# Kernel tuning notes

Measured on AMD Instinct MI355X. Metric: run time of the kernel, lower is better.

Reference implementation:

```python
import jax, jax.numpy as jnp
import numpy as np

N, LQ, D_MODEL, M_HEADS, P_POINTS, H_DIM, W_DIM = 8, 4096, 256, 8, 4, 64, 64


def setup_inputs() -> dict:
    key = jax.random.key(0)
    ks = jax.random.split(key, 9)
    d = D_MODEL
    scale = 1.0 / np.sqrt(d).astype(np.float32)
    return {
        "query": jax.random.normal(ks[0], (N, LQ, d), jnp.float32),
        "reference_points": jax.random.uniform(ks[1], (N, LQ, 2), jnp.float32),
        "input_flatten": jax.random.normal(ks[2], (N, H_DIM * W_DIM, d), jnp.float32),
        "H": H_DIM,
        "W": W_DIM,
        "Wv": jax.random.normal(ks[3], (d, d), jnp.float32) * scale,
        "bv": jnp.zeros((d,), jnp.float32),
        "Woff": jax.random.normal(ks[4], (M_HEADS * P_POINTS * 2, d), jnp.float32) * 0.01,
        "boff": jax.random.normal(ks[5], (M_HEADS * P_POINTS * 2,), jnp.float32) * 0.5,
        "Wa": jax.random.normal(ks[6], (M_HEADS * P_POINTS, d), jnp.float32) * 0.01,
        "ba": jnp.zeros((M_HEADS * P_POINTS,), jnp.float32),
        "Wo": jax.random.normal(ks[7], (d, d), jnp.float32) * scale,
        "bo": jnp.zeros((d,), jnp.float32),
    }


def _bilinear_sample(val, grid, H, W):
    # val: [B, D, H*W]; grid: [B, Lq, P, 2] in [-1, 1] (x, y); align_corners=False, zero padding.
    B, D, _ = val.shape
    _, Lq, P, _ = grid.shape
    x = (grid[..., 0] + 1.0) * (W * 0.5) - 0.5
    y = (grid[..., 1] + 1.0) * (H * 0.5) - 0.5
    x0 = jnp.floor(x)
    y0 = jnp.floor(y)
    x0i = x0.astype(jnp.int32)
    y0i = y0.astype(jnp.int32)
    wx1 = x - x0
    wy1 = y - y0
    out = jnp.zeros((B, D, Lq, P), val.dtype)
    for xi, wx in ((x0i, 1.0 - wx1), (x0i + 1, wx1)):
        for yi, wy in ((y0i, 1.0 - wy1), (y0i + 1, wy1)):
            valid = (xi >= 0) & (xi < W) & (yi >= 0) & (yi < H)
            idx = jnp.clip(yi, 0, H - 1) * W + jnp.clip(xi, 0, W - 1)  # [B, Lq, P]
            g = jnp.take_along_axis(val, idx.reshape(B, 1, Lq * P), axis=2).reshape(B, D, Lq, P)
            w = jnp.where(valid, wx * wy, 0.0)
            out = out + g * w[:, None]
    return out


def reference(query, reference_points, input_flatten, H, W, Wv, bv, Woff, boff, Wa, ba, Wo, bo):
    n, lq, d = query.shape
    m, p = M_HEADS, P_POINTS
    dh = d // m
    value = (input_flatten @ Wv.T + bv).reshape(n, H * W, m, dh)
    offsets = (query @ Woff.T + boff).reshape(n, lq, m, p, 2)
    attw = jax.nn.softmax((query @ Wa.T + ba).reshape(n, lq, m, p), axis=-1)
    normalizer = jnp.array([W, H], dtype=query.dtype)  # [W, H] order per torch code
    loc = reference_points[:, :, None, None, :] + offsets / normalizer
    grid = 2.0 * loc - 1.0  # [n, lq, m, p, 2]
    # value -> [n*m, dh, H*W] matching torch flatten(2).transpose(1,2).reshape
    val = jnp.transpose(value, (0, 2, 3, 1)).reshape(n * m, dh, H * W)
    grd = jnp.transpose(grid, (0, 2, 1, 3, 4)).reshape(n * m, lq, p, 2)
    samp = _bilinear_sample(val, grd, H, W)  # [n*m, dh, lq, p]
    aw = jnp.transpose(attw, (0, 2, 1, 3)).reshape(n * m, 1, lq, p)
    out = (samp * aw).sum(-1).reshape(n, m * dh, lq)
    out = jnp.transpose(out, (0, 2, 1))  # [n, lq, d]
    return out @ Wo.T + bo
```

## Files before the change

### kernel.cpp

```cpp
#include <hip/hip_runtime.h>
#include <math.h>

#define NB   8
#define LQN  4096
#define DM   256
#define MH   8
#define PP   4
#define HH   64
#define WW   64
#define PW   67
#define PPIX (PW*PW)

typedef __bf16 bf16x8 __attribute__((ext_vector_type(8)));
typedef float  f32x4  __attribute__((ext_vector_type(4)));
typedef unsigned short us8 __attribute__((ext_vector_type(8)));
typedef unsigned short us4 __attribute__((ext_vector_type(4)));

__device__ __forceinline__ unsigned short f2bf(float f) {
    unsigned u = __float_as_uint(f);
    u += 0x7FFFu + ((u >> 16) & 1u);
    return (unsigned short)(u >> 16);
}
__device__ __forceinline__ float bf2f(unsigned short b) {
    return __uint_as_float((unsigned)b << 16);
}

__device__ __forceinline__ void gl2lds16(const void* g, unsigned short* l) {
    __builtin_amdgcn_global_load_lds(
        (const __attribute__((address_space(1))) void*)g,
        (__attribute__((address_space(3))) void*)l,
        16, 0, 0);
}

__device__ __forceinline__ bf16x8 cvt_frag(const unsigned short* s, int row, int kq) {
    const int u0 = row * 8 + ((kq * 2) ^ (row & 7));
    const int u1 = u0 ^ 1;
    const f32x4 a0 = *(const f32x4*)&s[u0 * 8];
    const f32x4 a1 = *(const f32x4*)&s[u1 * 8];
    bf16x8 v;
    v[0] = (__bf16)a0[0]; v[1] = (__bf16)a0[1];
    v[2] = (__bf16)a0[2]; v[3] = (__bf16)a0[3];
    v[4] = (__bf16)a1[0]; v[5] = (__bf16)a1[1];
    v[6] = (__bf16)a1[2]; v[7] = (__bf16)a1[3];
    return v;
}

__global__ __launch_bounds__(256)
void prep_kernel(const float* __restrict__ Wv, const float* __restrict__ Wo,
                 const float* __restrict__ Woff, const float* __restrict__ Wa,
                 const float* __restrict__ boff, const float* __restrict__ ba,
                 unsigned short* __restrict__ Wvh, unsigned short* __restrict__ Woh,
                 unsigned short* __restrict__ Wcath, float* __restrict__ bcat,
                 unsigned short* __restrict__ valueP) {
    const int i = blockIdx.x * 256 + threadIdx.x;
    if (i < 65536) {
        Wvh[i] = f2bf(Wv[i]);
    } else if (i < 131072) {
        const int j = i - 65536;
        Woh[j] = f2bf(Wo[j]);
    } else if (i < 163840) {
        const int j = i - 131072, n = j >> 8, k = j & 255;
        const float v = (n < 64) ? Woff[n * 256 + k]
                                 : ((n < 96) ? Wa[(n - 64) * 256 + k] : 0.f);
        Wcath[j] = f2bf(v);
    } else if (i < 163968) {
        const int n = i - 163840;
        bcat[n] = (n < 64) ? boff[n] : ((n < 96) ? ba[n - 64] : 0.f);
    } else if (i < 163968 + 201216) {
        const int j   = i - 163968;
        const int c4  = j & 63;
        const int pix = j >> 6;
        const int n   = pix / 393;
        const int r   = pix - n * 393;
        int x, y;
        if (r < 201) {
            const int q = r / 67;
            y = (q == 0) ? 0 : (q == 1 ? 65 : 66);
            x = r - q * 67;
        } else {
            const int q = r - 201;
            y = 1 + q / 3;
            const int s = q - (q / 3) * 3;
            x = (s == 0) ? 0 : (s == 1 ? 65 : 66);
        }
        const size_t addr = ((size_t)n * PPIX + (size_t)y * PW + x) * DM + c4 * 4;
        *(ushort4*)&valueP[addr] = make_ushort4(0, 0, 0, 0);
    }
}

__global__ __launch_bounds__(256, 4)
void value_gemm(const float* __restrict__ Ain,
                const unsigned short* __restrict__ Wvh,
                const float* __restrict__ bv,
                unsigned short* __restrict__ valueP) {
    constexpr int K = 256, NK = 8;
    __shared__ unsigned short sA[2][4096];
    __shared__ unsigned short sB[2][4096];

    const int t   = threadIdx.x;
    const int blk = blockIdx.x;
    const int xb  = blk & 7;
    const int idx = blk >> 3;
    const int brow = xb * 4096 + (idx >> 1) * 64;
    const int bcol = (idx & 1) * 128;

    const int srow = t >> 3;
    const int scq  = (t & 7) ^ (srow & 7);
    const float* aG = Ain + (size_t)(brow + srow) * K + scq * 4;
    const size_t aI = (size_t)32 * K;

    const unsigned short* bG = Wvh + (size_t)(bcol + (t >> 2)) * K + (t & 3) * 8;
    const size_t bI = (size_t)64 * K;

    const int l   = t & 63;
    const int wid = t >> 6;
    const int wr  = wid >> 1, wc = wid & 1;
    const int fr  = l & 15,   kq = l >> 4;

    f32x4 acc[2][4] = {};

#define STAGE(buf, ks_) { const int k0_ = (ks_) * 32;                    \
       gl2lds16(aG + k0_,      &sA[buf][t * 8]);                         \
       gl2lds16(aG + k0_ + aI, &sA[buf][2048 + t * 8]);                  \
       gl2lds16(bG + k0_,      &sB[buf][t * 8]);                         \
       gl2lds16(bG + k0_ + bI, &sB[buf][2048 + t * 8]); }

    STAGE(0, 0);
    STAGE(1, 1);

    for (int ks = 0; ks < NK; ++ks) {
        const int cur = ks & 1;
        if (ks < NK - 1) asm volatile("s_waitcnt vmcnt(4)" ::: "memory");
        else             asm volatile("s_waitcnt vmcnt(0)" ::: "memory");
        __builtin_amdgcn_s_barrier();
        __builtin_amdgcn_sched_barrier(0);

        bf16x8 af[2], bf_[4];
#pragma unroll
        for (int m = 0; m < 2; ++m)
            af[m]  = cvt_frag(sA[cur], wr * 32 + m * 16 + fr, kq);
#pragma unroll
        for (int n = 0; n < 4; ++n)
            bf_[n] = *(const bf16x8*)&sB[cur][(wc * 64 + n * 16 + fr) * 32 + kq * 8];

#pragma unroll
        for (int m = 0; m < 2; ++m)
#pragma unroll
            for (int n = 0; n < 4; ++n)
                acc[m][n] = __builtin_amdgcn_mfma_f32_16x16x32_bf16(
                    bf_[n], af[m], acc[m][n], 0, 0, 0);

        __builtin_amdgcn_sched_barrier(0);
        __builtin_amdgcn_s_barrier();
        if (ks + 2 < NK) STAGE(cur, ks + 2);
    }
#undef STAGE

#pragma unroll
    for (int m = 0; m < 2; ++m) {
        const int row = brow + wr * 32 + m * 16 + fr;
        const int nb_ = row >> 12;
        const int pix = row & 4095;
        const int y   = pix >> 6, x = pix & 63;
        const size_t rbase =
            ((size_t)nb_ * PPIX + (size_t)(y + 1) * PW + (x + 1)) * DM;
#pragma unroll
        for (int n = 0; n < 4; ++n) {
            const int colq = bcol + wc * 64 + n * 16 + kq * 4;
            const float4 b4 = *(const float4*)&bv[colq];
            us4 o;
            o[0] = f2bf(acc[m][n][0] + b4.x);
            o[1] = f2bf(acc[m][n][1] + b4.y);
            o[2] = f2bf(acc[m][n][2] + b4.z);
            o[3] = f2bf(acc[m][n][3] + b4.w);
            *(us4*)&valueP[rbase + colq] = o;
        }
    }
}

__global__ __launch_bounds__(512, 4)
void fused_lso(const float* __restrict__ query, const float* __restrict__ refp,
               const unsigned short* __restrict__ valueP,
               const unsigned short* __restrict__ Wcath,
               const float* __restrict__ bcat,
               const unsigned short* __restrict__ Woh,
               const float* __restrict__ bo, float* __restrict__ C) {
    constexpr int K = 256, NK = 8;
    extern __shared__ unsigned short smem[];
    unsigned short* sS = smem;
    unsigned short* sB = smem + 16384;
    unsigned short* sL = smem + 32768;

    const int t    = threadIdx.x;
    const int blk  = blockIdx.x;
    const int nb   = blk & 7;
    const int brow = nb * 4096 + (blk >> 3) * 64;
    const int w    = t >> 6;
    const int lane = t & 63;
    const int fr   = lane & 15, kq = lane >> 4;

    {
        unsigned short* sQ = sS;
        unsigned short* sW = sS + 8192;

        const int srow = t >> 3;
        const int scq  = (t & 7) ^ (srow & 7);
        const float* aG = query + (size_t)(brow + srow) * K + scq * 4;
        const unsigned short* wG = Wcath + (size_t)(t >> 2) * K + (t & 3) * 8;

        const int wr0 = w >> 2;
        const int wc0 = w & 3;

        f32x4 acc[2][2] = {};

#define STG0(buf, ks_) { const int k0_ = (ks_) * 32;                     \
       gl2lds16(aG + k0_, &sQ[(buf) * 4096 + t * 8]);                    \
       gl2lds16(wG + k0_, &sW[(buf) * 4096 + t * 8]); }

        STG0(0, 0);
        STG0(1, 1);

        for (int ks = 0; ks < NK; ++ks) {
            const int cur = ks & 1;
            if (ks < NK - 1) asm volatile("s_waitcnt vmcnt(2)" ::: "memory");
            else             asm volatile("s_waitcnt vmcnt(0)" ::: "memory");
            __builtin_amdgcn_s_barrier();
            __builtin_amdgcn_sched_barrier(0);

            bf16x8 af[2], bw[2];
#pragma unroll
            for (int m = 0; m < 2; ++m)
                af[m] = cvt_frag(&sQ[cur * 4096], wr0 * 32 + m * 16 + fr, kq);
#pragma unroll
            for (int n = 0; n < 2; ++n)
                bw[n] = *(const bf16x8*)&sW[cur * 4096 +
                        (wc0 * 32 + n * 16 + fr) * 32 + kq * 8];

#pragma unroll
            for (int m = 0; m < 2; ++m)
#pragma unroll
                for (int n = 0; n < 2; ++n)
                    acc[m][n] = __builtin_amdgcn_mfma_f32_16x16x32_bf16(
                        bw[n], af[m], acc[m][n], 0, 0, 0);

            __builtin_amdgcn_sched_barrier(0);
            __builtin_amdgcn_s_barrier();
            if (ks + 2 < NK) STG0(cur, ks + 2);
        }
#undef STG0

#pragma unroll
        for (int m = 0; m < 2; ++m) {
            const int row = wr0 * 32 + m * 16 + fr;
#pragma unroll
            for (int n = 0; n < 2; ++n) {
                const int colq = wc0 * 32 + n * 16 + kq * 4;
                const float4 b4 = *(const float4*)&bcat[colq];
                us4 o;
                o[0] = f2bf(acc[m][n][0] + b4.x);
                o[1] = f2bf(acc[m][n][1] + b4.y);
                o[2] = f2bf(acc[m][n][2] + b4.z);
                o[3] = f2bf(acc[m][n][3] + b4.w);
                *(us4*)&sL[row * 128 + colq] = o;
            }
        }
    }
    __syncthreads();

    {
        const int tp  = lane & 31;
        const int pm  = tp >> 2, ppt = tp & 3;
        const int half = lane >> 5;
        const int c8   = lane & 31;
        const int mh   = c8 >> 2;
        const unsigned short* vbase = valueP + (size_t)nb * (PPIX * DM) + c8 * 8;

        for (int i = 0; i < 8; ++i) {
            const int q = w * 8 + i;
            const int b = brow + q;
            const unsigned short* lg = sL + q * 128;

            const float rx = refp[(size_t)b * 2 + 0];
            const float ry = refp[(size_t)b * 2 + 1];
            const float ox = bf2f(lg[pm * 8 + ppt * 2 + 0]);
            const float oy = bf2f(lg[pm * 8 + ppt * 2 + 1]);
            const float la = bf2f(lg[64 + tp]);

            const float x = fminf(fmaxf(fmaf(rx, (float)WW, ox) - 0.5f, -1.0f), 64.0f);
            const float y = fminf(fmaxf(fmaf(ry, (float)HH, oy) - 0.5f, -1.0f), 64.0f);

            float mx = fmaxf(la, __shfl_xor(la, 1));
            mx = fmaxf(mx, __shfl_xor(mx, 2));
            const float e = __expf(la - mx);
            float den = e + __shfl_xor(e, 1);
            den += __shfl_xor(den, 2);
            const float wgt = e / den;

            float accv[8] = {};
#pragma unroll
            for (int p = 0; p < PP; ++p) {
                const int   sl = mh * PP + p;
                const float xp = __shfl(x, sl);
                const float yp = __shfl(y, sl);
                const float wp = __shfl(wgt, sl);

                const float x0f = floorf(xp), y0f = floorf(yp);
                const int   x0 = (int)x0f,   y0 = (int)y0f;
                const float wx1 = xp - x0f,  wy1 = yp - y0f;
                const float wy  = half ? wy1 : (1.f - wy1);
                const float wA  = wp * wy * (1.f - wx1);
                const float wB  = wp * wy * wx1;

                const unsigned short* p0 =
                    vbase + (size_t)((y0 + 1 + half) * PW + (x0 + 1)) * DM;
                const us8 gA = *(const us8*)(p0);
                const us8 gB = *(const us8*)(p0 + DM);
#pragma unroll
                for (int j = 0; j < 8; ++j) {
                    accv[j] = fmaf(wA, bf2f(gA[j]), accv[j]);
                    accv[j] = fmaf(wB, bf2f(gB[j]), accv[j]);
                }
            }
#pragma unroll
            for (int j = 0; j < 8; ++j)
                accv[j] += __shfl_xor(accv[j], 32);

            if (half == 0) {
                us8 o;
#pragma unroll
                for (int j = 0; j < 8; ++j) o[j] = f2bf(accv[j]);
                *(us8*)&sS[q * 256 + ((c8 ^ (q & 7)) * 8)] = o;
            }
        }
    }
    __syncthreads();

    const unsigned short* bG = Woh + (size_t)(t >> 2) * K + (t & 3) * 8;
    const size_t rHalf = (size_t)128 * K;

    const int wr = w >> 2, wc = w & 3;

    f32x4 acc[2][4] = {};

#define STAGEF(buf, ks_) { const int k0_ = (ks_) * 32;                   \
       gl2lds16(bG + k0_,         &sB[(buf) * 8192 + t * 8]);            \
       gl2lds16(bG + k0_ + rHalf, &sB[(buf) * 8192 + 4096 + t * 8]); }

    STAGEF(0, 0);
    STAGEF(1, 1);

    for (int ks = 0; ks < NK; ++ks) {
        const int cur = ks & 1;
        if (ks < NK - 1) asm volatile("s_waitcnt vmcnt(2)" ::: "memory");
        else             asm volatile("s_waitcnt vmcnt(0)" ::: "memory");
        __builtin_amdgcn_s_barrier();
        __builtin_amdgcn_sched_barrier(0);

        bf16x8 af[2], bfr[4];
#pragma unroll
        for (int m = 0; m < 2; ++m) {
            const int row = wr * 32 + m * 16 + fr;
            const int u   = (ks * 4 + kq) ^ (row & 7);
            af[m] = *(const bf16x8*)&sS[row * 256 + u * 8];
        }
#pragma unroll
        for (int n = 0; n < 4; ++n)
            bfr[n] = *(const bf16x8*)&sB[cur * 8192 + (wc * 64 + n * 16 + fr) * 32 + kq * 8];

#pragma unroll
        for (int m = 0; m < 2; ++m)
#pragma unroll
            for (int n = 0; n < 4; ++n)
                acc[m][n] = __builtin_amdgcn_mfma_f32_16x16x32_bf16(
                    bfr[n], af[m], acc[m][n], 0, 0, 0);

        __builtin_amdgcn_sched_barrier(0);
        __builtin_amdgcn_s_barrier();
        if (ks + 2 < NK) STAGEF(cur, ks + 2);
    }
#undef STAGEF

#pragma unroll
    for (int m = 0; m < 2; ++m) {
        const int row = brow + wr * 32 + m * 16 + fr;
#pragma unroll
        for (int n = 0; n < 4; ++n) {
            const int colq = wc * 64 + n * 16 + kq * 4;
            const float4 bs = *(const float4*)&bo[colq];
            float4 o;
            o.x = acc[m][n][0] + bs.x; o.y = acc[m][n][1] + bs.y;
            o.z = acc[m][n][2] + bs.z; o.w = acc[m][n][3] + bs.w;
            *(float4*)&C[(size_t)row * DM + colq] = o;
        }
    }
}

extern "C" void kernel_launch(void* const* d_in, const int* in_sizes, int n_in,
                              void* d_out, int out_size, void* d_ws, size_t ws_size,
                              hipStream_t stream) {
    const float* query  = (const float*)d_in[0];
    const float* refp   = (const float*)d_in[1];
    const float* inputf = (const float*)d_in[2];
    const float* Wv   = (const float*)d_in[5];
    const float* bv   = (const float*)d_in[6];
    const float* Woff = (const float*)d_in[7];
    const float* boff = (const float*)d_in[8];
    const float* Wa   = (const float*)d_in[9];
    const float* ba   = (const float*)d_in[10];
    const float* Wo   = (const float*)d_in[11];
    const float* bo   = (const float*)d_in[12];
    float* out = (float*)d_out;

    unsigned short* valueP = (unsigned short*)d_ws;
    unsigned short* Wvh    = valueP + (size_t)NB * PPIX * DM;
    unsigned short* Woh    = Wvh    + 65536;
    unsigned short* Wcath  = Woh    + 65536;
    float*          bcat   = (float*)(Wcath + 32768);

    prep_kernel<<<1427, 256, 0, stream>>>(Wv, Wo, Woff, Wa, boff, ba,
                                          Wvh, Woh, Wcath, bcat, valueP);

    value_gemm<<<1024, 256, 0, stream>>>(inputf, Wvh, bv, valueP);

    fused_lso<<<512, 512, 81920, stream>>>(query, refp, valueP, Wcath, bcat,
                                           Woh, bo, out);
}
```

Baseline: 59.14 us.

## Halve rows per block and load GEMM operands directly from global memory

The fused kernel now handles 32 query rows per block instead of 64 and launches 1024 blocks. The projection and output GEMMs drop their LDS double-buffered staging and instead read query and weight fragments straight from global memory into MFMA registers, which shrinks dynamic shared memory from 80 KB to 24 KB. The aim is higher occupancy and fewer barriers. In exchange, weight tiles are re-read from global or L2 by more blocks, and uncoalesced per-lane fragment loads replace the staged copies.

```diff
diff --git a/kernel.cpp b/kernel.cpp
--- a/kernel.cpp
+++ b/kernel.cpp
@@ -185,84 +185,52 @@
                const float* __restrict__ bcat,
                const unsigned short* __restrict__ Woh,
                const float* __restrict__ bo, float* __restrict__ C) {
-    constexpr int K = 256, NK = 8;
     extern __shared__ unsigned short smem[];
     unsigned short* sS = smem;
-    unsigned short* sB = smem + 16384;
-    unsigned short* sL = smem + 32768;
+    unsigned short* sL = smem + 8192;
 
     const int t    = threadIdx.x;
     const int blk  = blockIdx.x;
     const int nb   = blk & 7;
-    const int brow = nb * 4096 + (blk >> 3) * 64;
+    const int brow = nb * 4096 + (blk >> 3) * 32;
     const int w    = t >> 6;
     const int lane = t & 63;
     const int fr   = lane & 15, kq = lane >> 4;
 
     {
-        unsigned short* sQ = sS;
-        unsigned short* sW = sS + 8192;
-
-        const int srow = t >> 3;
-        const int scq  = (t & 7) ^ (srow & 7);
-        const float* aG = query + (size_t)(brow + srow) * K + scq * 4;
-        const unsigned short* wG = Wcath + (size_t)(t >> 2) * K + (t & 3) * 8;
-
         const int wr0 = w >> 2;
         const int wc0 = w & 3;
-
-        f32x4 acc[2][2] = {};
-
-#define STG0(buf, ks_) { const int k0_ = (ks_) * 32;                     \
-       gl2lds16(aG + k0_, &sQ[(buf) * 4096 + t * 8]);                    \
-       gl2lds16(wG + k0_, &sW[(buf) * 4096 + t * 8]); }
-
-        STG0(0, 0);
-        STG0(1, 1);
-
-        for (int ks = 0; ks < NK; ++ks) {
-            const int cur = ks & 1;
-            if (ks < NK - 1) asm volatile("s_waitcnt vmcnt(2)" ::: "memory");
-            else             asm volatile("s_waitcnt vmcnt(0)" ::: "memory");
-            __builtin_amdgcn_s_barrier();
-            __builtin_amdgcn_sched_barrier(0);
-
-            bf16x8 af[2], bw[2];
-#pragma unroll
-            for (int m = 0; m < 2; ++m)
-                af[m] = cvt_frag(&sQ[cur * 4096], wr0 * 32 + m * 16 + fr, kq);
-#pragma unroll
-            for (int n = 0; n < 2; ++n)
-                bw[n] = *(const bf16x8*)&sW[cur * 4096 +
-                        (wc0 * 32 + n * 16 + fr) * 32 + kq * 8];
-
-#pragma unroll
-            for (int m = 0; m < 2; ++m)
-#pragma unroll
-                for (int n = 0; n < 2; ++n)
-                    acc[m][n] = __builtin_amdgcn_mfma_f32_16x16x32_bf16(
-                        bw[n], af[m], acc[m][n], 0, 0, 0);
-
-            __builtin_amdgcn_sched_barrier(0);
-            __builtin_amdgcn_s_barrier();
-            if (ks + 2 < NK) STG0(cur, ks + 2);
-        }
-#undef STG0
-
-#pragma unroll
-        for (int m = 0; m < 2; ++m) {
-            const int row = wr0 * 32 + m * 16 + fr;
-#pragma unroll
-            for (int n = 0; n < 2; ++n) {
-                const int colq = wc0 * 32 + n * 16 + kq * 4;
-                const float4 b4 = *(const float4*)&bcat[colq];
-                us4 o;
-                o[0] = f2bf(acc[m][n][0] + b4.x);
-                o[1] = f2bf(acc[m][n][1] + b4.y);
-                o[2] = f2bf(acc[m][n][2] + b4.z);
-                o[3] = f2bf(acc[m][n][3] + b4.w);
-                *(us4*)&sL[row * 128 + colq] = o;
-            }
+        const int qrow = wr0 * 16 + fr;
+        const float* aP = query + (size_t)(brow + qrow) * DM + kq * 8;
+        const unsigned short* b0 = Wcath + (size_t)(wc0 * 32 + fr) * DM + kq * 8;
+        const unsigned short* b1 = b0 + 16 * DM;
+
+        f32x4 acc[2] = {};
+#pragma unroll
+        for (int ks = 0; ks < 8; ++ks) {
+            const int k0 = ks * 32;
+            const f32x4 a0 = *(const f32x4*)(aP + k0);
+            const f32x4 a1 = *(const f32x4*)(aP + k0 + 4);
+            bf16x8 af;
+            af[0] = (__bf16)a0[0]; af[1] = (__bf16)a0[1];
+            af[2] = (__bf16)a0[2]; af[3] = (__bf16)a0[3];
+            af[4] = (__bf16)a1[0]; af[5] = (__bf16)a1[1];
+            af[6] = (__bf16)a1[2]; af[7] = (__bf16)a1[3];
+            const bf16x8 bw0 = *(const bf16x8*)(b0 + k0);
+            const bf16x8 bw1 = *(const bf16x8*)(b1 + k0);
+            acc[0] = __builtin_amdgcn_mfma_f32_16x16x32_bf16(bw0, af, acc[0], 0, 0, 0);
+            acc[1] = __builtin_amdgcn_mfma_f32_16x16x32_bf16(bw1, af, acc[1], 0, 0, 0);
+        }
+#pragma unroll
+        for (int n = 0; n < 2; ++n) {
+            const int colq = wc0 * 32 + n * 16 + kq * 4;
+            const float4 b4 = *(const float4*)&bcat[colq];
+            us4 o;
+            o[0] = f2bf(acc[n][0] + b4.x);
+            o[1] = f2bf(acc[n][1] + b4.y);
+            o[2] = f2bf(acc[n][2] + b4.z);
+            o[3] = f2bf(acc[n][3] + b4.w);
+            *(us4*)&sL[qrow * 128 + colq] = o;
         }
     }
     __syncthreads();
@@ -275,8 +243,8 @@
         const int mh   = c8 >> 2;
         const unsigned short* vbase = valueP + (size_t)nb * (PPIX * DM) + c8 * 8;
 
-        for (int i = 0; i < 8; ++i) {
-            const int q = w * 8 + i;
+        for (int i = 0; i < 4; ++i) {
+            const int q = w * 4 + i;
             const int b = brow + q;
             const unsigned short* lg = sL + q * 128;
 
@@ -335,62 +303,34 @@
     }
     __syncthreads();
 
-    const unsigned short* bG = Woh + (size_t)(t >> 2) * K + (t & 3) * 8;
-    const size_t rHalf = (size_t)128 * K;
-
-    const int wr = w >> 2, wc = w & 3;
-
-    f32x4 acc[2][4] = {};
-
-#define STAGEF(buf, ks_) { const int k0_ = (ks_) * 32;                   \
-       gl2lds16(bG + k0_,         &sB[(buf) * 8192 + t * 8]);            \
-       gl2lds16(bG + k0_ + rHalf, &sB[(buf) * 8192 + 4096 + t * 8]); }
-
-    STAGEF(0, 0);
-    STAGEF(1, 1);
-
-    for (int ks = 0; ks < NK; ++ks) {
-        const int cur = ks & 1;
-        if (ks < NK - 1) asm volatile("s_waitcnt vmcnt(2)" ::: "memory");
-        else             asm volatile("s_waitcnt vmcnt(0)" ::: "memory");
-        __builtin_amdgcn_s_barrier();
-        __builtin_amdgcn_sched_barrier(0);
-
-        bf16x8 af[2], bfr[4];
-#pragma unroll
-        for (int m = 0; m < 2; ++m) {
-            const int row = wr * 32 + m * 16 + fr;
-            const int u   = (ks * 4 + kq) ^ (row & 7);
-            af[m] = *(const bf16x8*)&sS[row * 256 + u * 8];
-        }
-#pragma unroll
-        for (int n = 0; n < 4; ++n)
-            bfr[n] = *(const bf16x8*)&sB[cur * 8192 + (wc * 64 + n * 16 + fr) * 32 + kq * 8];
-
-#pragma unroll
-        for (int m = 0; m < 2; ++m)
-#pragma unroll
-            for (int n = 0; n < 4; ++n)
-                acc[m][n] = __builtin_amdgcn_mfma_f32_16x16x32_bf16(
-                    bfr[n], af[m], acc[m][n], 0, 0, 0);
-
-        __builtin_amdgcn_sched_barrier(0);
-        __builtin_amdgcn_s_barrier();
-        if (ks + 2 < NK) STAGEF(cur, ks + 2);
-    }
-#undef STAGEF
-
-#pragma unroll
-    for (int m = 0; m < 2; ++m) {
-        const int row = brow + wr * 32 + m * 16 + fr;
+    {
+        const int wr2 = w >> 2;
+        const int wc2 = w & 3;
+        const int row = wr2 * 16 + fr;
+        const unsigned short* bP = Woh + (size_t)(wc2 * 64 + fr) * DM + kq * 8;
+
+        f32x4 acc[4] = {};
+#pragma unroll
+        for (int ks = 0; ks < 8; ++ks) {
+            const int k0 = ks * 32;
+            const bf16x8 af =
+                *(const bf16x8*)&sS[row * 256 + (((ks * 4 + kq) ^ (row & 7)) * 8)];
+#pragma unroll
+            for (int n = 0; n < 4; ++n) {
+                const bf16x8 bw = *(const bf16x8*)(bP + (size_t)n * 16 * DM + k0);
+                acc[n] = __builtin_amdgcn_mfma_f32_16x16x32_bf16(bw, af, acc[n], 0, 0, 0);
+            }
+        }
+
+        const int grow = brow + row;
 #pragma unroll
         for (int n = 0; n < 4; ++n) {
-            const int colq = wc * 64 + n * 16 + kq * 4;
+            const int colq = wc2 * 64 + n * 16 + kq * 4;
             const float4 bs = *(const float4*)&bo[colq];
             float4 o;
-            o.x = acc[m][n][0] + bs.x; o.y = acc[m][n][1] + bs.y;
-            o.z = acc[m][n][2] + bs.z; o.w = acc[m][n][3] + bs.w;
-            *(float4*)&C[(size_t)row * DM + colq] = o;
+            o.x = acc[n][0] + bs.x; o.y = acc[n][1] + bs.y;
+            o.z = acc[n][2] + bs.z; o.w = acc[n][3] + bs.w;
+            *(float4*)&C[(size_t)grow * DM + colq] = o;
         }
     }
 }
@@ -422,6 +362,6 @@
 
     value_gemm<<<1024, 256, 0, stream>>>(inputf, Wvh, bv, valueP);
 
-    fused_lso<<<512, 512, 81920, stream>>>(query, refp, valueP, Wcath, bcat,
-                                           Woh, bo, out);
-}
+    fused_lso<<<1024, 512, 24576, stream>>>(query, refp, valueP, Wcath, bcat,
+                                            Woh, bo, out);
+}
```

New measurement: 99.91 us. 68.9% more time.
